# Kernel tuning notes

Hardware: AMD Instinct MI355X
Metric: run time of the kernel (lower is better)

Reference implementation:

```python
import jax, jax.numpy as jnp
import numpy as np

BETA = 0.25  # commitment weight from config['beta']


def _mlp(h, ws, bs):
    # MLPLayers: Linear + ReLU between hidden layers, no activation after last.
    n = len(ws)
    for i in range(n):
        h = h @ ws[i] + bs[i]
        if i < n - 1:
            h = jax.nn.relu(h)
    return h


def setup_inputs() -> dict:
    key = jax.random.key(0)
    ks = jax.random.split(key, 16)
    B, IN = 65536, 768
    dims = [768, 512, 256, 128]  # [in_dim] + layers + [e_dim]
    d = {"x": jax.random.normal(ks[0], (B, IN), dtype=jnp.float32)}
    # encoder weights
    for i in range(3):
        fan_in = dims[i]
        d[f"enc_w{i}"] = jax.random.normal(ks[1 + i], (dims[i], dims[i + 1]), dtype=jnp.float32) / np.sqrt(fan_in)
        d[f"enc_b{i}"] = jnp.zeros((dims[i + 1],), dtype=jnp.float32)
    rdims = dims[::-1]
    for i in range(3):
        d[f"dec_w{i}"] = jax.random.normal(ks[4 + i], (rdims[i], rdims[i + 1]), dtype=jnp.float32) / np.sqrt(rdims[i])
        d[f"dec_b{i}"] = jnp.zeros((rdims[i + 1],), dtype=jnp.float32)
    # 4 residual levels, 256 codes each, e_dim=128
    d["codebooks"] = jax.random.normal(ks[7], (4, 256, 128), dtype=jnp.float32)
    return d


def reference(x, enc_w0, enc_b0, enc_w1, enc_b1, enc_w2, enc_b2,
              dec_w0, dec_b0, dec_w1, dec_b1, dec_w2, dec_b2, codebooks):
    sg = jax.lax.stop_gradient
    z = _mlp(x, [enc_w0, enc_w1, enc_w2], [enc_b0, enc_b1, enc_b2])  # (B, e_dim)

    residual = z
    x_q = jnp.zeros_like(z)
    losses = []
    n_levels = codebooks.shape[0]
    for l in range(n_levels):
        C = codebooks[l]  # (K, e_dim)
        # squared L2 distances (B, K) via expansion, avoids materializing diffs
        dist = (jnp.sum(residual * residual, axis=1, keepdims=True)
                - 2.0 * residual @ C.T
                + jnp.sum(C * C, axis=1))
        idx = jnp.argmin(dist, axis=1)  # (B,)
        q = C[idx]                      # (B, e_dim) gather
        # codebook loss + beta * commitment loss
        losses.append(jnp.mean((sg(q) - residual) ** 2)
                      + BETA * jnp.mean((q - sg(residual)) ** 2))
        x_q = x_q + q
        residual = residual - sg(q)
    rq_loss = jnp.mean(jnp.stack(losses))

    # straight-through estimator
    y_q = z + sg(x_q - z)
    y = _mlp(y_q, [dec_w0, dec_w1, dec_w2], [dec_b0, dec_b1, dec_b2])  # (B, in_dim)
    return y, rq_loss
```

## Files before the change

### kernel.cpp

```cpp
#include <hip/hip_runtime.h>
#include <cstdint>
#include <cstddef>


typedef _Float16 F16;
typedef F16   v8h  __attribute__((ext_vector_type(8)));
typedef F16   v2h  __attribute__((ext_vector_type(2)));
typedef F16   v4h  __attribute__((ext_vector_type(4)));
typedef float v4f  __attribute__((ext_vector_type(4)));

__device__ __forceinline__ void gload_lds16(const void* g, void* l) {
    __builtin_amdgcn_global_load_lds(
        (const __attribute__((address_space(1))) void*)g,
        (__attribute__((address_space(3))) void*)l, 16, 0, 0);
}

__device__ __forceinline__ void split2(float v, F16& h, F16& l) {
    h = (F16)v;
    l = (F16)((v - (float)h) * 2048.0f);
}

template<int OUT, bool RELU, bool HASBIAS>
__global__ __launch_bounds__(256, 2)
void f16gemm3(const F16* __restrict__ Ah, const F16* __restrict__ Al,
              const F16* __restrict__ Bh, const F16* __restrict__ Bl,
              const float* __restrict__ bias,
              float* __restrict__ C, F16* __restrict__ Ch, F16* __restrict__ Cl,
              const float* __restrict__ c2, float2* __restrict__ cand,
              int N, int K, int nbn)
{
    __shared__ __attribute__((aligned(16))) char smem[67584];
    v8h* As = (v8h*)smem;
    v8h* Bs = (v8h*)(smem + 32768);

    const int tid  = threadIdx.x;
    const int lane = tid & 63;
    const int wid  = tid >> 6;

    const int cpx = gridDim.x >> 3;
    const int sw  = (blockIdx.x & 7) * cpx + (blockIdx.x >> 3);
    const int mt  = sw / nbn;
    const int nt_ = sw - mt * nbn;
    const long bm = (long)mt * 128;
    const long bn = (long)nt_ * 128;

    const int rr = lane >> 3;
    const int c  = (lane & 7) ^ rr;
    const F16* aS[4]; const F16* bS[4];
    int dOf[4];
    #pragma unroll
    for (int jj = 0; jj < 4; jj++) {
        int rloc = wid * 32 + jj * 8;
        long ag = bm + rloc + rr, bg = bn + rloc + rr;
        aS[jj] = (c < 4) ? (Ah + ag * (long)K + c * 8) : (Al + ag * (long)K + (c - 4) * 8);
        bS[jj] = (c < 4) ? (Bh + bg * (long)K + c * 8) : (Bl + bg * (long)K + (c - 4) * 8);
        dOf[jj] = rloc * 8;
    }

    const int cq = lane >> 4;
    const int wr = wid >> 1, wc = wid & 1;
    int aOff[4], bOff[4];
    #pragma unroll
    for (int i = 0; i < 4; i++) {
        int am  = wr * 64 + i * 16 + (lane & 15);
        aOff[i] = am * 8 + (cq ^ (am & 7));
        int bn2 = wc * 64 + i * 16 + (lane & 15);
        bOff[i] = bn2 * 8 + (cq ^ (bn2 & 7));
    }

    v4f acc[4][4]  = {};
    v4f accx[4][4] = {};

    auto stage = [&](int buf, int k0) {
        v8h* Ab = As + buf * 1024;
        v8h* Bb = Bs + buf * 1024;
        #pragma unroll
        for (int jj = 0; jj < 4; jj++) gload_lds16(aS[jj] + k0, Ab + dOf[jj]);
        #pragma unroll
        for (int jj = 0; jj < 4; jj++) gload_lds16(bS[jj] + k0, Bb + dOf[jj]);
    };

    const int nsteps = K >> 5;
    stage(0, 0);

    for (int t = 0; t < nsteps; ++t) {
        const int cur = t & 1;
        if (t + 1 < nsteps) {
            stage(cur ^ 1, (t + 1) * 32);
            asm volatile("s_waitcnt vmcnt(8)" ::: "memory");
        } else {
            asm volatile("s_waitcnt vmcnt(0)" ::: "memory");
        }
        __builtin_amdgcn_sched_barrier(0);
        __builtin_amdgcn_s_barrier();
        __builtin_amdgcn_sched_barrier(0);

        const v8h* Ab = As + cur * 1024;
        const v8h* Bb = Bs + cur * 1024;
        v8h ah[4], al[4], bh[4], bl[4];
        #pragma unroll
        for (int i = 0; i < 4; i++) {
            ah[i] = Ab[aOff[i]]; al[i] = Ab[aOff[i] ^ 4];
            bh[i] = Bb[bOff[i]]; bl[i] = Bb[bOff[i] ^ 4];
        }
        __builtin_amdgcn_s_setprio(1);
        #pragma unroll
        for (int mi = 0; mi < 4; mi++)
            #pragma unroll
            for (int ni = 0; ni < 4; ni++) {
                acc[mi][ni]  = __builtin_amdgcn_mfma_f32_16x16x32_f16(ah[mi], bh[ni], acc[mi][ni],  0, 0, 0);
                accx[mi][ni] = __builtin_amdgcn_mfma_f32_16x16x32_f16(ah[mi], bl[ni], accx[mi][ni], 0, 0, 0);
                accx[mi][ni] = __builtin_amdgcn_mfma_f32_16x16x32_f16(al[mi], bh[ni], accx[mi][ni], 0, 0, 0);
            }
        __builtin_amdgcn_s_setprio(0);
        __builtin_amdgcn_sched_barrier(0);
        __builtin_amdgcn_s_barrier();
        __builtin_amdgcn_sched_barrier(0);
    }

    const int cl = lane & 15;
    const int rb = (lane >> 4) * 4;

    if constexpr (OUT == 3) {
        float* cD = (float*)smem;
        int*   cI = (int*)(smem + 1024);
        float bd[4][4]; int bi[4][4];
        #pragma unroll
        for (int mi = 0; mi < 4; mi++)
            #pragma unroll
            for (int r = 0; r < 4; r++) {
                float bb = 3.4e38f; int ii = 0;
                #pragma unroll
                for (int ni = 0; ni < 4; ni++) {
                    int code = (int)bn + wc * 64 + ni * 16 + cl;
                    float s  = acc[mi][ni][r] + accx[mi][ni][r] * (1.0f / 2048.0f);
                    float d  = fmaf(-2.0f, s, c2[code]);
                    if (d < bb || (d == bb && code < ii)) { bb = d; ii = code; }
                }
                bd[mi][r] = bb; bi[mi][r] = ii;
            }
        #pragma unroll
        for (int off = 1; off < 16; off <<= 1)
            #pragma unroll
            for (int mi = 0; mi < 4; mi++)
                #pragma unroll
                for (int r = 0; r < 4; r++) {
                    float od = __shfl_xor(bd[mi][r], off);
                    int   oi = __shfl_xor(bi[mi][r], off);
                    if (od < bd[mi][r] || (od == bd[mi][r] && oi < bi[mi][r])) {
                        bd[mi][r] = od; bi[mi][r] = oi;
                    }
                }
        if (cl == 0)
            #pragma unroll
            for (int mi = 0; mi < 4; mi++)
                #pragma unroll
                for (int r = 0; r < 4; r++) {
                    int rl = wr * 64 + mi * 16 + rb + r;
                    cD[rl * 2 + wc] = bd[mi][r];
                    cI[rl * 2 + wc] = bi[mi][r];
                }
        __syncthreads();
        if (tid < 128) {
            float d0 = cD[tid * 2], d1 = cD[tid * 2 + 1];
            int   i0 = cI[tid * 2], i1 = cI[tid * 2 + 1];
            float pd; int pk;
            if (d1 < d0 || (d1 == d0 && i1 < i0)) { pd = d1; pk = i1; }
            else                                  { pd = d0; pk = i0; }
            float2 out; out.x = pd; out.y = __int_as_float(pk);
            cand[(bm + tid) * 2 + (bn >> 7)] = out;
        }
    } else {
        float* sC = (float*)smem;
        #pragma unroll
        for (int mi = 0; mi < 4; mi++)
            #pragma unroll
            for (int ni = 0; ni < 4; ni++)
                #pragma unroll
                for (int r = 0; r < 4; r++)
                    sC[(wr * 64 + mi * 16 + rb + r) * 132 + wc * 64 + ni * 16 + cl] =
                        acc[mi][ni][r] + accx[mi][ni][r] * (1.0f / 2048.0f);
        __syncthreads();
        const int trow = tid >> 5;
        const int tcol = (tid & 31) << 2;
        float4 bv = {0.f, 0.f, 0.f, 0.f};
        if constexpr (HASBIAS) bv = *reinterpret_cast<const float4*>(bias + bn + tcol);
        #pragma unroll
        for (int it = 0; it < 16; ++it) {
            int row = trow + it * 8;
            float4 v = *reinterpret_cast<const float4*>(&sC[row * 132 + tcol]);
            v.x += bv.x; v.y += bv.y; v.z += bv.z; v.w += bv.w;
            if constexpr (RELU) {
                v.x = fmaxf(v.x, 0.f); v.y = fmaxf(v.y, 0.f);
                v.z = fmaxf(v.z, 0.f); v.w = fmaxf(v.w, 0.f);
            }
            long gr = (bm + row) * (long)N + bn + tcol;
            if constexpr (OUT == 0 || OUT == 2)
                *reinterpret_cast<float4*>(C + gr) = v;
            if constexpr (OUT == 1 || OUT == 2) {
                v4h h4, l4; F16 h, l;
                split2(v.x, h, l); h4[0] = h; l4[0] = l;
                split2(v.y, h, l); h4[1] = h; l4[1] = l;
                split2(v.z, h, l); h4[2] = h; l4[2] = l;
                split2(v.w, h, l); h4[3] = h; l4[3] = l;
                *reinterpret_cast<v4h*>(Ch + gr) = h4;
                *reinterpret_cast<v4h*>(Cl + gr) = l4;
            }
        }
    }
}

__device__ __forceinline__ void wprep_task(const float* __restrict__ W,
                                           F16* __restrict__ H, F16* __restrict__ L,
                                           int K, int N, int idx, int stride, int total)
{
    for (int i = idx; i < total; i += stride) {
        int k = i / N, n = i - k * N;
        float v = W[i];
        F16 h, l; split2(v, h, l);
        H[(long)n * K + k] = h;
        L[(long)n * K + k] = l;
    }
}

__global__ __launch_bounds__(256)
void prep_all(const float* __restrict__ x,
              const float* __restrict__ ew0, const float* __restrict__ ew1,
              const float* __restrict__ ew2, const float* __restrict__ dw0,
              const float* __restrict__ dw1, const float* __restrict__ cball,
              F16* __restrict__ Xh, F16* __restrict__ Xl,
              F16* __restrict__ e0h, F16* __restrict__ e0l,
              F16* __restrict__ e1h, F16* __restrict__ e1l,
              F16* __restrict__ e2h, F16* __restrict__ e2l,
              F16* __restrict__ d0h, F16* __restrict__ d0l,
              F16* __restrict__ d1h, F16* __restrict__ d1l,
              F16* __restrict__ cbh, F16* __restrict__ cbl,
              float* __restrict__ c2all, float* __restrict__ F)
{
    const int b = blockIdx.x, t = threadIdx.x;
    if (b < 3072) {
        for (long i = (long)b * 256 + t; i < 12582912; i += 786432) {
            float4 v = reinterpret_cast<const float4*>(x)[i];
            v4h h4, l4; F16 h, l;
            split2(v.x, h, l); h4[0] = h; l4[0] = l;
            split2(v.y, h, l); h4[1] = h; l4[1] = l;
            split2(v.z, h, l); h4[2] = h; l4[2] = l;
            split2(v.w, h, l); h4[3] = h; l4[3] = l;
            reinterpret_cast<v4h*>(Xh)[i] = h4;
            reinterpret_cast<v4h*>(Xl)[i] = l4;
        }
    } else if (b < 3584) wprep_task(ew0, e0h, e0l, 768, 512, (b - 3072) * 256 + t, 131072, 393216);
    else if (b < 3712)   wprep_task(ew1, e1h, e1l, 512, 256, (b - 3584) * 256 + t, 32768, 131072);
    else if (b < 3744)   wprep_task(ew2, e2h, e2l, 256, 128, (b - 3712) * 256 + t, 8192, 32768);
    else if (b < 3776)   wprep_task(dw0, d0h, d0l, 128, 256, (b - 3744) * 256 + t, 8192, 32768);
    else if (b < 3904)   wprep_task(dw1, d1h, d1l, 256, 512, (b - 3776) * 256 + t, 32768, 131072);
    else if (b < 4032) {
        for (int i = (b - 3904) * 256 + t; i < 131072; i += 32768) {
            float v = cball[i];
            F16 h, l; split2(v, h, l);
            cbh[i] = h; cbl[i] = l;
        }
    } else if (b < 4036) {
        int i = (b - 4032) * 256 + t;
        const float* row = cball + (long)i * 128;
        float s = 0.f;
        #pragma unroll
        for (int d = 0; d < 128; d += 4) {
            float4 v = *reinterpret_cast<const float4*>(row + d);
            s += v.x * v.x + v.y * v.y + v.z * v.z + v.w * v.w;
        }
        c2all[i] = s;
    } else {
        if (t < 4) F[t] = 0.f;
    }
}

__global__ void wprep_kernel(const float* __restrict__ W, F16* __restrict__ H,
                             F16* __restrict__ L, int K, int N)
{
    int i = blockIdx.x * 256 + threadIdx.x;
    if (i >= K * N) return;
    wprep_task(W, H, L, K, N, i, K * N, i + 1);
}

__global__ __launch_bounds__(256)
void rq_update2(const float2* __restrict__ cand,
                const float* __restrict__ cb,
                const float* __restrict__ src,
                float* __restrict__ resid,
                F16* __restrict__ residh, F16* __restrict__ residl,
                float* __restrict__ xq,
                F16* __restrict__ xqh, F16* __restrict__ xql,
                float* __restrict__ lossF,
                int M, int first, int last)
{
    __shared__ float lsum[4];
    const int tid  = threadIdx.x;
    const int lane = tid & 63;
    const int wave = tid >> 6;

    float myloss = 0.f;
    const int stride = gridDim.x * 4;
    for (int row = blockIdx.x * 4 + wave; row < M; row += stride) {
        float2 c0 = cand[(long)row * 2];
        float2 c1 = cand[(long)row * 2 + 1];
        int i0 = __float_as_int(c0.y), i1 = __float_as_int(c1.y);
        int bidx = (c1.x < c0.x || (c1.x == c0.x && i1 < i0)) ? i1 : i0;

        long base = (long)row * 128 + lane * 2;
        float2 r = *reinterpret_cast<const float2*>(src + base);
        float2 q = *reinterpret_cast<const float2*>(cb + (long)bidx * 128 + lane * 2);
        float dx = r.x - q.x, dy = r.y - q.y;
        myloss += dx * dx + dy * dy;

        if (!last) {
            float2 nr; nr.x = dx; nr.y = dy;
            *reinterpret_cast<float2*>(resid + base) = nr;
            v2h nh, nl; F16 h, l;
            split2(dx, h, l); nh[0] = h; nl[0] = l;
            split2(dy, h, l); nh[1] = h; nl[1] = l;
            *reinterpret_cast<v2h*>(residh + base) = nh;
            *reinterpret_cast<v2h*>(residl + base) = nl;
        }
        float2 xv;
        if (first) { xv.x = q.x; xv.y = q.y; }
        else {
            xv = *reinterpret_cast<float2*>(xq + base);
            xv.x += q.x; xv.y += q.y;
        }
        if (!last) {
            *reinterpret_cast<float2*>(xq + base) = xv;
        } else {
            v2h nh, nl; F16 h, l;
            split2(xv.x, h, l); nh[0] = h; nl[0] = l;
            split2(xv.y, h, l); nh[1] = h; nl[1] = l;
            *reinterpret_cast<v2h*>(xqh + base) = nh;
            *reinterpret_cast<v2h*>(xql + base) = nl;
        }
    }

    #pragma unroll
    for (int off = 32; off > 0; off >>= 1) myloss += __shfl_down(myloss, off);
    if (lane == 0) lsum[wave] = myloss;
    __syncthreads();
    if (tid == 0) atomicAdd(lossF, (lsum[0] + lsum[1]) + (lsum[2] + lsum[3]));
}

__global__ void finalize_loss_kernel(const float* __restrict__ F, float* __restrict__ out)
{
    if (threadIdx.x == 0) {
        float s = (F[0] + F[1]) + (F[2] + F[3]);
        out[0] = s * (1.25f / (4.f * 65536.f * 128.f));
    }
}

extern "C" void kernel_launch(void* const* d_in, const int* in_sizes, int n_in,
                              void* d_out, int out_size, void* d_ws, size_t ws_size,
                              hipStream_t stream)
{
    const float* x      = (const float*)d_in[0];
    const float* enc_w0 = (const float*)d_in[1];
    const float* enc_b0 = (const float*)d_in[2];
    const float* enc_w1 = (const float*)d_in[3];
    const float* enc_b1 = (const float*)d_in[4];
    const float* enc_w2 = (const float*)d_in[5];
    const float* enc_b2 = (const float*)d_in[6];
    const float* dec_w0 = (const float*)d_in[7];
    const float* dec_b0 = (const float*)d_in[8];
    const float* dec_w1 = (const float*)d_in[9];
    const float* dec_b1 = (const float*)d_in[10];
    const float* dec_w2 = (const float*)d_in[11];
    const float* dec_b2 = (const float*)d_in[12];
    const float* codebooks = (const float*)d_in[13];

    const int M = 65536;

    F16*   wsF = (F16*)d_ws;
    float* wsf = (float*)d_ws;
    F16*   Xh  = wsF;
    F16*   Xl  = wsF + 50331648;
    float* z   = wsf;
    F16*   zh  = wsF + 16777216;
    F16*   zl  = wsF + 25165824;
    F16*   g2l = wsF;
    F16*   g2h = wsF + 33554432;
    F16*   h2h = wsF + 67108864;
    F16*   h2l = wsF + 83886080;
    F16*   g1h = wsF + 67108864;
    F16*   g1l = wsF + 83886080;
    F16*   d2h = wsF + 67108864;
    F16*   d2l = d2h + 393216;

    F16*   doF = (F16*)d_out;
    float* y   = (float*)d_out;
    F16*   h1h = doF;
    F16*   h1l = doF + 33554432;
    float* xq  = (float*)d_out;
    F16*   xqh = doF + 16777216;
    F16*   xql = doF + 25165824;
    F16* e0h = doF + 67108864;  F16* e0l = e0h + 393216;
    F16* e1h = e0l + 393216;    F16* e1l = e1h + 131072;
    F16* e2h = e1l + 131072;    F16* e2l = e2h + 32768;
    F16* d0h = e2l + 32768;     F16* d0l = d0h + 32768;
    F16* d1h = d0l + 32768;     F16* d1l = d1h + 131072;
    F16* cbh = d1l + 131072;    F16* cbl = cbh + 131072;
    float2* cand  = (float2*)(doF + 68812800);
    float*  c2all = (float*)(doF + 69337088);
    float*  F     = c2all + 1024;

    dim3 blk(256);

    prep_all<<<dim3(4037), blk, 0, stream>>>(x, enc_w0, enc_w1, enc_w2, dec_w0, dec_w1,
                                             codebooks, Xh, Xl, e0h, e0l, e1h, e1l,
                                             e2h, e2l, d0h, d0l, d1h, d1l, cbh, cbl,
                                             c2all, F);

    f16gemm3<1, true,  true><<<dim3(2048), blk, 0, stream>>>(Xh, Xl, e0h, e0l, enc_b0, nullptr, h1h, h1l, nullptr, nullptr, 512, 768, 4);
    f16gemm3<1, true,  true><<<dim3(1024), blk, 0, stream>>>(h1h, h1l, e1h, e1l, enc_b1, nullptr, h2h, h2l, nullptr, nullptr, 256, 512, 2);
    f16gemm3<2, false, true><<<dim3(512),  blk, 0, stream>>>(h2h, h2l, e2h, e2l, enc_b2, z, zh, zl, nullptr, nullptr, 128, 256, 1);

    for (int l = 0; l < 4; l++) {
        const float* cb = codebooks + (long)l * 32768;
        f16gemm3<3, false, false><<<dim3(1024), blk, 0, stream>>>(zh, zl, cbh + l * 32768, cbl + l * 32768,
                                                                  nullptr, nullptr, nullptr, nullptr,
                                                                  c2all + l * 256, cand, 256, 128, 2);
        rq_update2<<<dim3(1024), blk, 0, stream>>>(cand, cb, z, z, zh, zl, xq, xqh, xql,
                                                   F + l, M, (l == 0) ? 1 : 0, (l == 3) ? 1 : 0);
    }
    finalize_loss_kernel<<<dim3(1), dim3(64), 0, stream>>>(F, y + 50331648);

    f16gemm3<1, true,  true><<<dim3(1024), blk, 0, stream>>>(xqh, xql, d0h, d0l, dec_b0, nullptr, g1h, g1l, nullptr, nullptr, 256, 128, 2);
    f16gemm3<1, true,  true><<<dim3(2048), blk, 0, stream>>>(g1h, g1l, d1h, d1l, dec_b1, nullptr, g2h, g2l, nullptr, nullptr, 512, 256, 4);
    wprep_kernel<<<dim3(1536), blk, 0, stream>>>(dec_w2, d2h, d2l, 512, 768);
    f16gemm3<0, false, true><<<dim3(3072), blk, 0, stream>>>(g2h, g2l, d2h, d2l, dec_b2, y, nullptr, nullptr, nullptr, nullptr, 768, 512, 6);
}
```

Measured before the change: 1.147 ms.

## Interleave LDS fragment loads with MFMA clusters and drop fp32 residual/xq traffic

The GEMM inner loop now loads A/B fragments in stages and issues MFMAs in 2x2 clusters between the loads, so LDS reads overlap with matrix math. The RQ update kernel stops keeping separate fp32 residual and x_q buffers. It rebuilds the residual from the fp16 hi/lo split and recovers x_q at the last level as z minus the final residual, which cuts global memory reads and writes per level. The residual now carries split-fp16 precision (about 22 bits), and x_q = z - r may differ slightly from the summed codes.

```diff
diff --git a/kernel.cpp b/kernel.cpp
--- a/kernel.cpp
+++ b/kernel.cpp
@@ -19,6 +19,17 @@
     h = (F16)v;
     l = (F16)((v - (float)h) * 2048.0f);
 }
+
+#define MFMA3(mi, ni) \
+    acc[mi][ni]  = __builtin_amdgcn_mfma_f32_16x16x32_f16(ah[mi], bh[ni], acc[mi][ni],  0, 0, 0); \
+    accx[mi][ni] = __builtin_amdgcn_mfma_f32_16x16x32_f16(ah[mi], bl[ni], accx[mi][ni], 0, 0, 0); \
+    accx[mi][ni] = __builtin_amdgcn_mfma_f32_16x16x32_f16(al[mi], bh[ni], accx[mi][ni], 0, 0, 0);
+
+#define CLUSTER(ma, mb, na, nb) \
+    __builtin_amdgcn_s_setprio(1); \
+    MFMA3(ma, na) MFMA3(ma, nb) MFMA3(mb, na) MFMA3(mb, nb) \
+    __builtin_amdgcn_s_setprio(0); \
+    __builtin_amdgcn_sched_barrier(0);
 
 template<int OUT, bool RELU, bool HASBIAS>
 __global__ __launch_bounds__(256, 2)
@@ -98,22 +109,21 @@
         const v8h* Ab = As + cur * 1024;
         const v8h* Bb = Bs + cur * 1024;
         v8h ah[4], al[4], bh[4], bl[4];
-        #pragma unroll
-        for (int i = 0; i < 4; i++) {
-            ah[i] = Ab[aOff[i]]; al[i] = Ab[aOff[i] ^ 4];
-            bh[i] = Bb[bOff[i]]; bl[i] = Bb[bOff[i] ^ 4];
-        }
-        __builtin_amdgcn_s_setprio(1);
-        #pragma unroll
-        for (int mi = 0; mi < 4; mi++)
-            #pragma unroll
-            for (int ni = 0; ni < 4; ni++) {
-                acc[mi][ni]  = __builtin_amdgcn_mfma_f32_16x16x32_f16(ah[mi], bh[ni], acc[mi][ni],  0, 0, 0);
-                accx[mi][ni] = __builtin_amdgcn_mfma_f32_16x16x32_f16(ah[mi], bl[ni], accx[mi][ni], 0, 0, 0);
-                accx[mi][ni] = __builtin_amdgcn_mfma_f32_16x16x32_f16(al[mi], bh[ni], accx[mi][ni], 0, 0, 0);
-            }
-        __builtin_amdgcn_s_setprio(0);
-        __builtin_amdgcn_sched_barrier(0);
+        ah[0] = Ab[aOff[0]]; al[0] = Ab[aOff[0] ^ 4];
+        ah[1] = Ab[aOff[1]]; al[1] = Ab[aOff[1] ^ 4];
+        bh[0] = Bb[bOff[0]]; bl[0] = Bb[bOff[0] ^ 4];
+        bh[1] = Bb[bOff[1]]; bl[1] = Bb[bOff[1] ^ 4];
+        __builtin_amdgcn_sched_barrier(0);
+        bh[2] = Bb[bOff[2]]; bl[2] = Bb[bOff[2] ^ 4];
+        bh[3] = Bb[bOff[3]]; bl[3] = Bb[bOff[3] ^ 4];
+        __builtin_amdgcn_sched_barrier(0);
+        CLUSTER(0, 1, 0, 1)
+        ah[2] = Ab[aOff[2]]; al[2] = Ab[aOff[2] ^ 4];
+        ah[3] = Ab[aOff[3]]; al[3] = Ab[aOff[3] ^ 4];
+        __builtin_amdgcn_sched_barrier(0);
+        CLUSTER(0, 1, 2, 3)
+        CLUSTER(2, 3, 0, 1)
+        CLUSTER(2, 3, 2, 3)
         __builtin_amdgcn_s_barrier();
         __builtin_amdgcn_sched_barrier(0);
     }
@@ -284,15 +294,13 @@
 }
 
 __global__ __launch_bounds__(256)
-void rq_update2(const float2* __restrict__ cand,
+void rq_update3(const float2* __restrict__ cand,
                 const float* __restrict__ cb,
-                const float* __restrict__ src,
-                float* __restrict__ resid,
-                F16* __restrict__ residh, F16* __restrict__ residl,
-                float* __restrict__ xq,
+                F16* __restrict__ rh, F16* __restrict__ rl,
+                const float* __restrict__ z,
                 F16* __restrict__ xqh, F16* __restrict__ xql,
                 float* __restrict__ lossF,
-                int M, int first, int last)
+                int M, int last)
 {
     __shared__ float lsum[4];
     const int tid  = threadIdx.x;
@@ -308,32 +316,24 @@
         int bidx = (c1.x < c0.x || (c1.x == c0.x && i1 < i0)) ? i1 : i0;
 
         long base = (long)row * 128 + lane * 2;
-        float2 r = *reinterpret_cast<const float2*>(src + base);
+        v2h hr = *reinterpret_cast<const v2h*>(rh + base);
+        v2h lr = *reinterpret_cast<const v2h*>(rl + base);
+        float rx = (float)hr[0] + (float)lr[0] * (1.0f / 2048.0f);
+        float ry = (float)hr[1] + (float)lr[1] * (1.0f / 2048.0f);
         float2 q = *reinterpret_cast<const float2*>(cb + (long)bidx * 128 + lane * 2);
-        float dx = r.x - q.x, dy = r.y - q.y;
+        float dx = rx - q.x, dy = ry - q.y;
         myloss += dx * dx + dy * dy;
 
+        v2h nh, nl; F16 h, l;
         if (!last) {
-            float2 nr; nr.x = dx; nr.y = dy;
-            *reinterpret_cast<float2*>(resid + base) = nr;
-            v2h nh, nl; F16 h, l;
             split2(dx, h, l); nh[0] = h; nl[0] = l;
             split2(dy, h, l); nh[1] = h; nl[1] = l;
-            *reinterpret_cast<v2h*>(residh + base) = nh;
-            *reinterpret_cast<v2h*>(residl + base) = nl;
-        }
-        float2 xv;
-        if (first) { xv.x = q.x; xv.y = q.y; }
-        else {
-            xv = *reinterpret_cast<float2*>(xq + base);
-            xv.x += q.x; xv.y += q.y;
-        }
-        if (!last) {
-            *reinterpret_cast<float2*>(xq + base) = xv;
+            *reinterpret_cast<v2h*>(rh + base) = nh;
+            *reinterpret_cast<v2h*>(rl + base) = nl;
         } else {
-            v2h nh, nl; F16 h, l;
-            split2(xv.x, h, l); nh[0] = h; nl[0] = l;
-            split2(xv.y, h, l); nh[1] = h; nl[1] = l;
+            float2 zv = *reinterpret_cast<const float2*>(z + base);
+            split2(zv.x - dx, h, l); nh[0] = h; nl[0] = l;
+            split2(zv.y - dy, h, l); nh[1] = h; nl[1] = l;
             *reinterpret_cast<v2h*>(xqh + base) = nh;
             *reinterpret_cast<v2h*>(xql + base) = nl;
         }
@@ -395,7 +395,6 @@
     float* y   = (float*)d_out;
     F16*   h1h = doF;
     F16*   h1l = doF + 33554432;
-    float* xq  = (float*)d_out;
     F16*   xqh = doF + 16777216;
     F16*   xql = doF + 25165824;
     F16* e0h = doF + 67108864;  F16* e0l = e0h + 393216;
@@ -424,8 +423,8 @@
         f16gemm3<3, false, false><<<dim3(1024), blk, 0, stream>>>(zh, zl, cbh + l * 32768, cbl + l * 32768,
                                                                   nullptr, nullptr, nullptr, nullptr,
                                                                   c2all + l * 256, cand, 256, 128, 2);
-        rq_update2<<<dim3(1024), blk, 0, stream>>>(cand, cb, z, z, zh, zl, xq, xqh, xql,
-                                                   F + l, M, (l == 0) ? 1 : 0, (l == 3) ? 1 : 0);
+        rq_update3<<<dim3(1024), blk, 0, stream>>>(cand, cb, zh, zl, z, xqh, xql,
+                                                   F + l, M, (l == 3) ? 1 : 0);
     }
     finalize_loss_kernel<<<dim3(1), dim3(64), 0, stream>>>(F, y + 50331648);
 
```

New measurement: 1.120 ms. 2.4% less time.
